# Kernel optimization log

Measured on AMD Instinct MI355X. Metric: run time of the kernel, lower is better.

Reference implementation:

```python
import jax, jax.numpy as jnp
import numpy as np

N = 50000
E = 400000
IN_DIM = 256
H1 = 512
H2 = 128
P_DROP = 0.5


def setup_inputs() -> dict:
    key = jax.random.key(0)
    ks = jax.random.split(key, 8)
    x = jax.random.normal(ks[0], (N, IN_DIM), dtype=jnp.float32)
    edge_index = jax.random.randint(ks[1], (2, E), 0, N, dtype=jnp.int64)
    W1 = jax.random.normal(ks[2], (IN_DIM, H1), dtype=jnp.float32) * (1.0 / np.sqrt(IN_DIM))
    b1 = jnp.zeros((H1,), dtype=jnp.float32)
    W2 = jax.random.normal(ks[3], (H1, H2), dtype=jnp.float32) * (1.0 / np.sqrt(H1))
    b2 = jnp.zeros((H2,), dtype=jnp.float32)
    a = jnp.full((1,), 0.25, dtype=jnp.float32)  # PReLU default init
    mask1 = jax.random.bernoulli(ks[4], 1.0 - P_DROP, (N, H1))
    mask2 = jax.random.bernoulli(ks[5], 1.0 - P_DROP, (N, H2))
    return {"x": x, "edge_index": edge_index, "W1": W1, "b1": b1,
            "W2": W2, "b2": b2, "a": a, "mask1": mask1, "mask2": mask2}


def reference(x, edge_index, W1, b1, W2, b2, a, mask1, mask2):
    n = x.shape[0]
    loop = jnp.arange(n, dtype=edge_index.dtype)
    src = jnp.concatenate([edge_index[0], loop])  # [E+N] with self-loops
    dst = jnp.concatenate([edge_index[1], loop])
    # symmetric normalization: deg^-1/2[src] * deg^-1/2[dst]
    deg = jax.ops.segment_sum(jnp.ones(src.shape[0], x.dtype), dst, num_segments=n)
    dis = jnp.where(deg > 0, jax.lax.rsqrt(jnp.maximum(deg, 1.0)), 0.0)
    norm = dis[src] * dis[dst]  # [E+N]

    scale = 1.0 / (1.0 - P_DROP)

    def gcn_conv(h, W, b):
        h = h @ W                               # dense transform [n, out]
        msg = h[src] * norm[:, None]            # gather + normalize [E+N, out]
        return jax.ops.segment_sum(msg, dst, num_segments=n) + b

    def prelu_dropout(h, mask):
        h = jnp.where(h >= 0, h, a * h)         # PReLU (shared scalar a)
        return jnp.where(mask, h * scale, 0.0)  # dropout p=0.5

    feat1 = prelu_dropout(gcn_conv(x, W1, b1), mask1)
    feat2 = prelu_dropout(gcn_conv(feat1, W2, b2), mask2)
    return feat2
```

## Files before the change

kernel.cpp:

```cpp
#include <hip/hip_runtime.h>
#include <hip/hip_bf16.h>

#define IN_DIM 256
#define H1 512
#define H2 128
#define BM 128
#define BKK 64
#define LDT 72
#define SCAN_CHUNK 4096

typedef unsigned short u16;
typedef unsigned long long u64;
typedef __attribute__((ext_vector_type(8))) short short8;
typedef __attribute__((ext_vector_type(4))) float floatx4;

__device__ __forceinline__ u16 f2bf(float f) {
    union { float f; unsigned u; } c; c.f = f;
    unsigned u = c.u;
    return (u16)((u + 0x7fffu + ((u >> 16) & 1u)) >> 16);
}
__device__ __forceinline__ float bflo(unsigned w) {
    union { unsigned u; float f; } c; c.u = w << 16; return c.f;
}
__device__ __forceinline__ float bfhi(unsigned w) {
    union { unsigned u; float f; } c; c.u = w & 0xffff0000u; return c.f;
}


__global__ __launch_bounds__(256) void pack_mask_kernel(const int4* __restrict__ mask4,
        u64* __restrict__ bits, int total4) {
    int gid = blockIdx.x * blockDim.x + threadIdx.x;
    int lane = threadIdx.x & 63;
    int4 v = (gid < total4) ? mask4[gid] : make_int4(0, 0, 0, 0);
    u64 b0 = __ballot(v.x != 0);
    u64 b1 = __ballot(v.y != 0);
    u64 b2 = __ballot(v.z != 0);
    u64 b3 = __ballot(v.w != 0);
    u64 sel = (lane == 0) ? b0 : (lane == 1) ? b1 : (lane == 2) ? b2 : b3;
    if (lane < 4 && gid < total4)
        bits[(size_t)(gid >> 6) * 4 + lane] = sel;
}


__global__ void hist_kernel(const int* __restrict__ dstA, int* __restrict__ counts,
                            int E, int n) {
    int e = blockIdx.x * blockDim.x + threadIdx.x;
    if (e < E) {
        int d = dstA[e];
        if ((unsigned)d < (unsigned)n) atomicAdd(&counts[d], 1);
    }
}


__global__ __launch_bounds__(256) void partial_sum_kernel(const int* __restrict__ counts,
        int* __restrict__ partials, int n) {
    int t = threadIdx.x;
    int base = blockIdx.x * SCAN_CHUNK + t * 16;
    int s = 0;
    int m = (base < n) ? min(16, n - base) : 0;
    for (int i = 0; i < m; ++i) s += counts[base + i];
    __shared__ int red[256];
    red[t] = s;
    __syncthreads();
    for (int off = 128; off > 0; off >>= 1) {
        if (t < off) red[t] += red[t + off];
        __syncthreads();
    }
    if (t == 0) partials[blockIdx.x] = red[0];
}

__global__ void scan_partials_kernel(int* __restrict__ partials, int nb) {
    if (threadIdx.x == 0 && blockIdx.x == 0) {
        int run = 0;
        for (int i = 0; i < nb; ++i) { int c = partials[i]; partials[i] = run; run += c; }
        partials[nb] = run;
    }
}

__global__ __launch_bounds__(256) void scan_emit_kernel(const int* __restrict__ counts,
        const int* __restrict__ partials, int* __restrict__ row_start,
        int* __restrict__ cursor, float* __restrict__ dis, int n, int nb) {
    int t = threadIdx.x;
    int base = blockIdx.x * SCAN_CHUNK + t * 16;
    int cnt[16];
    int s = 0;
    int m = (base < n) ? min(16, n - base) : 0;
    for (int i = 0; i < m; ++i) { cnt[i] = counts[base + i]; s += cnt[i]; }
    __shared__ int red[256];
    red[t] = s;
    __syncthreads();
    for (int off = 1; off < 256; off <<= 1) {
        int v = red[t];
        int vo = (t >= off) ? red[t - off] : 0;
        __syncthreads();
        red[t] = v + vo;
        __syncthreads();
    }
    int run = partials[blockIdx.x] + (t ? red[t - 1] : 0);
    for (int i = 0; i < m; ++i) {
        int c = cnt[i];
        row_start[base + i] = run;
        cursor[base + i] = run;
        dis[base + i] = rsqrtf((float)(c + 1));
        run += c;
    }
    if (blockIdx.x == 0 && t == 0) row_start[n] = partials[nb];
}

__global__ void scatter_kernel(const int* __restrict__ srcA, const int* __restrict__ dstA,
                               int* __restrict__ cursor, int* __restrict__ csr,
                               int E, int n) {
    int e = blockIdx.x * blockDim.x + threadIdx.x;
    if (e < E) {
        int d = dstA[e];
        int s = srcA[e];
        if ((unsigned)d < (unsigned)n && (unsigned)s < (unsigned)n) {
            int p = atomicAdd(&cursor[d], 1);
            csr[p] = s;
        }
    }
}

__global__ void scale_cast_kernel(const float* __restrict__ x, const float* __restrict__ dis,
                                  u16* __restrict__ xs, int n) {
    int gid = blockIdx.x * blockDim.x + threadIdx.x;
    int total = n * (IN_DIM / 4);
    if (gid >= total) return;
    int node = gid >> 6;
    float4 v = ((const float4*)x)[gid];
    float d = dis[node];
    uint2 o;
    o.x = (unsigned)f2bf(v.x * d) | ((unsigned)f2bf(v.y * d) << 16);
    o.y = (unsigned)f2bf(v.z * d) | ((unsigned)f2bf(v.w * d) << 16);
    ((uint2*)xs)[gid] = o;
}

__global__ void transpose_cast_kernel(const float* __restrict__ W, u16* __restrict__ Wt,
                                      int K, int Ncols) {
    int idx = blockIdx.x * blockDim.x + threadIdx.x;
    if (idx >= K * Ncols) return;
    int k = idx / Ncols, c = idx - k * Ncols;
    Wt[c * K + k] = f2bf(W[idx]);
}


__global__ __launch_bounds__(256) void agg1_kernel(const u16* __restrict__ xs,
        const int* __restrict__ row_start, const int* __restrict__ csr,
        const float* __restrict__ dis, u16* __restrict__ aggx, int n) {
    int gid = blockIdx.x * blockDim.x + threadIdx.x;
    int w = gid >> 6, lane = gid & 63;
    if (w >= n) return;
    const uint2* base = (const uint2*)xs;
    uint2 v = base[(size_t)w * 64 + lane];
    float a0 = bflo(v.x), a1 = bfhi(v.x), a2 = bflo(v.y), a3 = bfhi(v.y);
    int b = row_start[w], e = row_start[w + 1];
    int i = b;
    for (; i + 4 <= e; i += 4) {
        int s0 = csr[i], s1 = csr[i + 1], s2 = csr[i + 2], s3 = csr[i + 3];
        uint2 u0 = base[(size_t)s0 * 64 + lane];
        uint2 u1 = base[(size_t)s1 * 64 + lane];
        uint2 u2 = base[(size_t)s2 * 64 + lane];
        uint2 u3 = base[(size_t)s3 * 64 + lane];
        a0 += (bflo(u0.x) + bflo(u1.x)) + (bflo(u2.x) + bflo(u3.x));
        a1 += (bfhi(u0.x) + bfhi(u1.x)) + (bfhi(u2.x) + bfhi(u3.x));
        a2 += (bflo(u0.y) + bflo(u1.y)) + (bflo(u2.y) + bflo(u3.y));
        a3 += (bfhi(u0.y) + bfhi(u1.y)) + (bfhi(u2.y) + bfhi(u3.y));
    }
    for (; i < e; ++i) {
        int s = csr[i];
        uint2 u = base[(size_t)s * 64 + lane];
        a0 += bflo(u.x); a1 += bfhi(u.x); a2 += bflo(u.y); a3 += bfhi(u.y);
    }
    float dd = dis[w];
    uint2 o;
    o.x = (unsigned)f2bf(a0 * dd) | ((unsigned)f2bf(a1 * dd) << 16);
    o.y = (unsigned)f2bf(a2 * dd) | ((unsigned)f2bf(a3 * dd) << 16);
    ((uint2*)aggx)[(size_t)w * 64 + lane] = o;
}


__global__ __launch_bounds__(256) void gemm1_kernel(const u16* __restrict__ A,
        const u16* __restrict__ Bt, const float* __restrict__ bias,
        const float* __restrict__ a_p, const u64* __restrict__ mbits,
        u16* __restrict__ out, int M) {
    const int K = IN_DIM;
    __shared__ __align__(16) u16 As[BM * LDT];
    __shared__ __align__(16) u16 Bs[BM * LDT];
    int tid = threadIdx.x;
    int wave = tid >> 6, lane = tid & 63;
    int quad = lane >> 4, l16 = lane & 15;
    int wm = wave & 1, wn = wave >> 1;
    int m0 = blockIdx.x * BM, n0 = blockIdx.y * BM;

    floatx4 acc[4][4];
#pragma unroll
    for (int i = 0; i < 4; i++)
#pragma unroll
        for (int j = 0; j < 4; j++) acc[i][j] = (floatx4){0.f, 0.f, 0.f, 0.f};

    for (int k0 = 0; k0 < K; k0 += BKK) {
        __syncthreads();
#pragma unroll
        for (int u = tid; u < 1024; u += 256) {
            int row = u >> 3, seg = u & 7;
            uint4 av = make_uint4(0, 0, 0, 0);
            int gr = m0 + row;
            if (gr < M) av = *(const uint4*)&A[(size_t)gr * K + k0 + seg * 8];
            *(uint4*)&As[row * LDT + seg * 8] = av;
            uint4 bv = *(const uint4*)&Bt[(size_t)(n0 + row) * K + k0 + seg * 8];
            *(uint4*)&Bs[row * LDT + seg * 8] = bv;
        }
        __syncthreads();
        short8 bf8[4][2];
#pragma unroll
        for (int i = 0; i < 4; i++)
#pragma unroll
            for (int ks = 0; ks < 2; ks++)
                bf8[i][ks] = *(const short8*)&Bs[(wn * 64 + i * 16 + l16) * LDT + ks * 32 + quad * 8];
#pragma unroll
        for (int mt = 0; mt < 4; mt++) {
            short8 af0 = *(const short8*)&As[(wm * 64 + mt * 16 + l16) * LDT + quad * 8];
            short8 af1 = *(const short8*)&As[(wm * 64 + mt * 16 + l16) * LDT + 32 + quad * 8];
#pragma unroll
            for (int nt = 0; nt < 4; nt++) {
                acc[mt][nt] = __builtin_amdgcn_mfma_f32_16x16x32_bf16(
                    af0, bf8[nt][0], acc[mt][nt], 0, 0, 0);
                acc[mt][nt] = __builtin_amdgcn_mfma_f32_16x16x32_bf16(
                    af1, bf8[nt][1], acc[mt][nt], 0, 0, 0);
            }
        }
    }

    u64* mb = (u64*)As;
    __syncthreads();
    for (int u = tid; u < BM * 4; u += 256) {
        int row = u >> 2, j = u & 3;
        int gr = m0 + row;
        u64 val = 0;
        if (gr < M) val = mbits[(size_t)gr * 8 + (n0 >> 8) * 4 + j];
        mb[row * 5 + j] = val;
    }
    __syncthreads();

    float alpha = a_p[0];
#pragma unroll
    for (int mt = 0; mt < 4; mt++) {
#pragma unroll
        for (int r = 0; r < 4; r++) {
            int lr = wm * 64 + mt * 16 + quad * 4 + r;
            int row = m0 + lr;
            if (row >= M) continue;
#pragma unroll
            for (int nt = 0; nt < 4; nt++) {
                int c64 = nt * 16 + l16;
                int col = n0 + wn * 64 + c64;
                float v = acc[mt][nt][r] + bias[col];
                v = (v >= 0.f) ? v : alpha * v;
                u64 w = mb[lr * 5 + (l16 & 3)];
                int bit = ((n0 >> 2) + wn * 16 + nt * 4 + (l16 >> 2)) & 63;
                v = ((w >> bit) & 1ull) ? v * 2.0f : 0.0f;
                out[(size_t)row * H1 + col] = f2bf(v);
            }
        }
    }
}


__global__ __launch_bounds__(256) void gemm2_kernel(const u16* __restrict__ A,
        const u16* __restrict__ Bt, const float* __restrict__ dis,
        u16* __restrict__ out, int M) {
    const int K = H1;
    __shared__ __align__(16) u16 As[64 * LDT];
    __shared__ __align__(16) u16 Bs[128 * LDT];
    int tid = threadIdx.x;
    int wave = tid >> 6, lane = tid & 63;
    int quad = lane >> 4, l16 = lane & 15;
    int wm = wave & 1, wn = wave >> 1;
    int m0 = blockIdx.x * 64;

    floatx4 acc[2][4];
#pragma unroll
    for (int i = 0; i < 2; i++)
#pragma unroll
        for (int j = 0; j < 4; j++) acc[i][j] = (floatx4){0.f, 0.f, 0.f, 0.f};

    for (int k0 = 0; k0 < K; k0 += BKK) {
        __syncthreads();
#pragma unroll
        for (int u = tid; u < 1536; u += 256) {
            if (u < 512) {
                int row = u >> 3, seg = u & 7;
                uint4 av = make_uint4(0, 0, 0, 0);
                int gr = m0 + row;
                if (gr < M) av = *(const uint4*)&A[(size_t)gr * K + k0 + seg * 8];
                *(uint4*)&As[row * LDT + seg * 8] = av;
            } else {
                int v2 = u - 512;
                int row = v2 >> 3, seg = v2 & 7;
                uint4 bv = *(const uint4*)&Bt[(size_t)row * K + k0 + seg * 8];
                *(uint4*)&Bs[row * LDT + seg * 8] = bv;
            }
        }
        __syncthreads();
        short8 bf8[4][2];
#pragma unroll
        for (int i = 0; i < 4; i++)
#pragma unroll
            for (int ks = 0; ks < 2; ks++)
                bf8[i][ks] = *(const short8*)&Bs[(wn * 64 + i * 16 + l16) * LDT + ks * 32 + quad * 8];
#pragma unroll
        for (int mt = 0; mt < 2; mt++) {
            short8 af0 = *(const short8*)&As[(wm * 32 + mt * 16 + l16) * LDT + quad * 8];
            short8 af1 = *(const short8*)&As[(wm * 32 + mt * 16 + l16) * LDT + 32 + quad * 8];
#pragma unroll
            for (int nt = 0; nt < 4; nt++) {
                acc[mt][nt] = __builtin_amdgcn_mfma_f32_16x16x32_bf16(
                    af0, bf8[nt][0], acc[mt][nt], 0, 0, 0);
                acc[mt][nt] = __builtin_amdgcn_mfma_f32_16x16x32_bf16(
                    af1, bf8[nt][1], acc[mt][nt], 0, 0, 0);
            }
        }
    }

#pragma unroll
    for (int mt = 0; mt < 2; mt++) {
#pragma unroll
        for (int r = 0; r < 4; r++) {
            int row = m0 + wm * 32 + mt * 16 + quad * 4 + r;
            if (row >= M) continue;
            float dd = dis[row];
#pragma unroll
            for (int nt = 0; nt < 4; nt++) {
                int col = wn * 64 + nt * 16 + l16;
                out[(size_t)row * H2 + col] = f2bf(acc[mt][nt][r] * dd);
            }
        }
    }
}


__global__ __launch_bounds__(256) void agg2_kernel(const u16* __restrict__ ts,
        const int* __restrict__ row_start, const int* __restrict__ csr,
        const float* __restrict__ dis, const float* __restrict__ b2,
        const float* __restrict__ a_p, const int* __restrict__ mask,
        float* __restrict__ out, int n) {
    int gid = blockIdx.x * blockDim.x + threadIdx.x;
    int w = gid >> 6, lane = gid & 63;
    if (w >= n) return;
    const unsigned* base = (const unsigned*)ts;
    unsigned v = base[(size_t)w * 64 + lane];
    float a0 = bflo(v), a1 = bfhi(v);
    int b = row_start[w], e = row_start[w + 1];
    int i = b;
    for (; i + 4 <= e; i += 4) {
        int s0 = csr[i], s1 = csr[i + 1], s2 = csr[i + 2], s3 = csr[i + 3];
        unsigned u0 = base[(size_t)s0 * 64 + lane];
        unsigned u1 = base[(size_t)s1 * 64 + lane];
        unsigned u2 = base[(size_t)s2 * 64 + lane];
        unsigned u3 = base[(size_t)s3 * 64 + lane];
        a0 += (bflo(u0) + bflo(u1)) + (bflo(u2) + bflo(u3));
        a1 += (bfhi(u0) + bfhi(u1)) + (bfhi(u2) + bfhi(u3));
    }
    for (; i < e; ++i) {
        int s = csr[i];
        unsigned u = base[(size_t)s * 64 + lane];
        a0 += bflo(u); a1 += bfhi(u);
    }
    float dd = dis[w];
    float alpha = a_p[0];
    int c0 = lane * 2;
    float v0 = dd * a0 + b2[c0];
    float v1 = dd * a1 + b2[c0 + 1];
    v0 = (v0 >= 0.f) ? v0 : alpha * v0;
    v1 = (v1 >= 0.f) ? v1 : alpha * v1;
    int2 m = ((const int2*)mask)[(size_t)w * 64 + lane];
    v0 = m.x ? v0 * 2.f : 0.f;
    v1 = m.y ? v1 * 2.f : 0.f;
    ((float2*)out)[(size_t)w * 64 + lane] = make_float2(v0, v1);
}


extern "C" void kernel_launch(void* const* d_in, const int* in_sizes, int n_in,
                              void* d_out, int out_size, void* d_ws, size_t ws_size,
                              hipStream_t stream) {
    const float* x  = (const float*)d_in[0];
    const int* ei   = (const int*)d_in[1];
    const float* W1 = (const float*)d_in[2];
    const float* b1 = (const float*)d_in[3];
    const float* W2 = (const float*)d_in[4];
    const float* b2 = (const float*)d_in[5];
    const float* ap = (const float*)d_in[6];
    const int* mask1 = (const int*)d_in[7];
    const int* mask2 = (const int*)d_in[8];

    int n = in_sizes[0] / IN_DIM;
    int E = in_sizes[1] / 2;
    const int* srcA = ei;
    const int* dstA = ei + E;

    char* p = (char*)d_ws;
    auto alloc = [&](size_t bytes) {
        char* r = p;
        p += (bytes + 255) & ~(size_t)255;
        return r;
    };
    u16* feat1     = (u16*)alloc((size_t)n * H1 * 2);
    u16* xs        = feat1;
    u16* ts        = (u16*)alloc((size_t)n * H2 * 2);
    u64* bits1     = (u64*)ts;
    u16* w1t       = (u16*)alloc((size_t)IN_DIM * H1 * 2);
    u16* w2t       = (u16*)alloc((size_t)H1 * H2 * 2);
    float* dis     = (float*)alloc((size_t)n * 4);
    int* counts    = (int*)alloc((size_t)n * 4);
    int* cursor    = (int*)alloc((size_t)n * 4);
    int* row_start = (int*)alloc(((size_t)n + 1) * 4);
    int* csr       = (int*)alloc((size_t)E * 4);
    int nscan = (n + SCAN_CHUNK - 1) / SCAN_CHUNK;
    int* partials  = (int*)alloc(((size_t)nscan + 1) * 4);
    u16* aggx      = (u16*)d_out;
    if ((size_t)(p - (char*)d_ws) > ws_size) return;

    const int tpb = 256;
    int total4 = n * H1 / 4;
    hipMemsetAsync(counts, 0, (size_t)n * 4, stream);
    pack_mask_kernel<<<(total4 + tpb - 1) / tpb, tpb, 0, stream>>>((const int4*)mask1,
        bits1, total4);
    hist_kernel<<<(E + tpb - 1) / tpb, tpb, 0, stream>>>(dstA, counts, E, n);
    partial_sum_kernel<<<nscan, tpb, 0, stream>>>(counts, partials, n);
    scan_partials_kernel<<<1, 64, 0, stream>>>(partials, nscan);
    scan_emit_kernel<<<nscan, tpb, 0, stream>>>(counts, partials, row_start, cursor, dis, n, nscan);
    scatter_kernel<<<(E + tpb - 1) / tpb, tpb, 0, stream>>>(srcA, dstA, cursor, csr, E, n);
    scale_cast_kernel<<<((n * (IN_DIM / 4)) + tpb - 1) / tpb, tpb, 0, stream>>>(x, dis, xs, n);
    transpose_cast_kernel<<<((IN_DIM * H1) + tpb - 1) / tpb, tpb, 0, stream>>>(W1, w1t, IN_DIM, H1);
    transpose_cast_kernel<<<((H1 * H2) + tpb - 1) / tpb, tpb, 0, stream>>>(W2, w2t, H1, H2);
    agg1_kernel<<<(n * 64 + tpb - 1) / tpb, tpb, 0, stream>>>(xs, row_start, csr, dis, aggx, n);
    dim3 g1((n + BM - 1) / BM, H1 / BM);
    gemm1_kernel<<<g1, tpb, 0, stream>>>(aggx, w1t, b1, ap, bits1, feat1, n);
    dim3 g2((n + 63) / 64, 1);
    gemm2_kernel<<<g2, tpb, 0, stream>>>(feat1, w2t, dis, ts, n);
    agg2_kernel<<<(n * 64 + tpb - 1) / tpb, tpb, 0, stream>>>(ts, row_start, csr, dis, b2, ap,
                                                              mask2, (float*)d_out, n);
}
```

Baseline: 416.5 us.

## Split waves across two edges with wider gathers; pad CSR rows to even length

Both aggregation kernels now have each half-wave gather a different neighbor row. Lanes use 16-byte (agg1) or 8-byte (agg2) loads, and the two halves are combined with a cross-half shuffle at the end. To support this, every CSR row is padded to an even length, with the pad entry pointing at an extra all-zero row appended to the bf16 feature buffers. Separately, mask packing, the degree histogram and both weight transpose-casts are merged into one multi-role prep kernel to cut launch count. The risk is the extra padded gathers and the half-wave store path.

```diff
diff --git a/kernel.cpp b/kernel.cpp
--- a/kernel.cpp
+++ b/kernel.cpp
@@ -27,27 +27,42 @@
 }
 
 
-__global__ __launch_bounds__(256) void pack_mask_kernel(const int4* __restrict__ mask4,
-        u64* __restrict__ bits, int total4) {
-    int gid = blockIdx.x * blockDim.x + threadIdx.x;
-    int lane = threadIdx.x & 63;
-    int4 v = (gid < total4) ? mask4[gid] : make_int4(0, 0, 0, 0);
-    u64 b0 = __ballot(v.x != 0);
-    u64 b1 = __ballot(v.y != 0);
-    u64 b2 = __ballot(v.z != 0);
-    u64 b3 = __ballot(v.w != 0);
-    u64 sel = (lane == 0) ? b0 : (lane == 1) ? b1 : (lane == 2) ? b2 : b3;
-    if (lane < 4 && gid < total4)
-        bits[(size_t)(gid >> 6) * 4 + lane] = sel;
-}
-
-
-__global__ void hist_kernel(const int* __restrict__ dstA, int* __restrict__ counts,
-                            int E, int n) {
-    int e = blockIdx.x * blockDim.x + threadIdx.x;
-    if (e < E) {
-        int d = dstA[e];
-        if ((unsigned)d < (unsigned)n) atomicAdd(&counts[d], 1);
+__global__ __launch_bounds__(256) void prep_kernel(const int4* __restrict__ mask4,
+        u64* __restrict__ bits, int total4,
+        const int* __restrict__ dstA, int* __restrict__ counts, int E, int n,
+        const float* __restrict__ W1, u16* __restrict__ w1t,
+        const float* __restrict__ W2, u16* __restrict__ w2t,
+        int PB, int HB, int T1B) {
+    int b = blockIdx.x;
+    if (b < PB) {
+        int gid = b * 256 + threadIdx.x;
+        int lane = threadIdx.x & 63;
+        int4 v = (gid < total4) ? mask4[gid] : make_int4(0, 0, 0, 0);
+        u64 b0 = __ballot(v.x != 0);
+        u64 b1 = __ballot(v.y != 0);
+        u64 b2 = __ballot(v.z != 0);
+        u64 b3 = __ballot(v.w != 0);
+        u64 sel = (lane == 0) ? b0 : (lane == 1) ? b1 : (lane == 2) ? b2 : b3;
+        if (lane < 4 && gid < total4)
+            bits[(size_t)(gid >> 6) * 4 + lane] = sel;
+    } else if (b < PB + HB) {
+        int e = (b - PB) * 256 + threadIdx.x;
+        if (e < E) {
+            int d = dstA[e];
+            if ((unsigned)d < (unsigned)n) atomicAdd(&counts[d], 1);
+        }
+    } else if (b < PB + HB + T1B) {
+        int idx = (b - PB - HB) * 256 + threadIdx.x;
+        if (idx < IN_DIM * H1) {
+            int k = idx >> 9, c = idx & (H1 - 1);
+            w1t[c * IN_DIM + k] = f2bf(W1[idx]);
+        }
+    } else {
+        int idx = (b - PB - HB - T1B) * 256 + threadIdx.x;
+        if (idx < H1 * H2) {
+            int k = idx >> 7, c = idx & (H2 - 1);
+            w2t[c * H1 + k] = f2bf(W2[idx]);
+        }
     }
 }
 
@@ -58,7 +73,7 @@
     int base = blockIdx.x * SCAN_CHUNK + t * 16;
     int s = 0;
     int m = (base < n) ? min(16, n - base) : 0;
-    for (int i = 0; i < m; ++i) s += counts[base + i];
+    for (int i = 0; i < m; ++i) s += (counts[base + i] + 1) & ~1;
     __shared__ int red[256];
     red[t] = s;
     __syncthreads();
@@ -69,8 +84,11 @@
     if (t == 0) partials[blockIdx.x] = red[0];
 }
 
-__global__ void scan_partials_kernel(int* __restrict__ partials, int nb) {
-    if (threadIdx.x == 0 && blockIdx.x == 0) {
+__global__ void scan_partials_kernel(int* __restrict__ partials, int nb,
+                                     unsigned* __restrict__ ts_zero_row) {
+    int t = threadIdx.x;
+    if (t < 64) ts_zero_row[t] = 0;
+    if (t == 0 && blockIdx.x == 0) {
         int run = 0;
         for (int i = 0; i < nb; ++i) { int c = partials[i]; partials[i] = run; run += c; }
         partials[nb] = run;
@@ -79,13 +97,14 @@
 
 __global__ __launch_bounds__(256) void scan_emit_kernel(const int* __restrict__ counts,
         const int* __restrict__ partials, int* __restrict__ row_start,
-        int* __restrict__ cursor, float* __restrict__ dis, int n, int nb) {
+        int* __restrict__ cursor, float* __restrict__ dis,
+        int* __restrict__ csr, int n, int nb) {
     int t = threadIdx.x;
     int base = blockIdx.x * SCAN_CHUNK + t * 16;
     int cnt[16];
     int s = 0;
     int m = (base < n) ? min(16, n - base) : 0;
-    for (int i = 0; i < m; ++i) { cnt[i] = counts[base + i]; s += cnt[i]; }
+    for (int i = 0; i < m; ++i) { cnt[i] = counts[base + i]; s += (cnt[i] + 1) & ~1; }
     __shared__ int red[256];
     red[t] = s;
     __syncthreads();
@@ -102,7 +121,8 @@
         row_start[base + i] = run;
         cursor[base + i] = run;
         dis[base + i] = rsqrtf((float)(c + 1));
-        run += c;
+        if (c & 1) csr[run + c] = n;
+        run += (c + 1) & ~1;
     }
     if (blockIdx.x == 0 && t == 0) row_start[n] = partials[nb];
 }
@@ -124,23 +144,17 @@
 __global__ void scale_cast_kernel(const float* __restrict__ x, const float* __restrict__ dis,
                                   u16* __restrict__ xs, int n) {
     int gid = blockIdx.x * blockDim.x + threadIdx.x;
-    int total = n * (IN_DIM / 4);
+    int total = (n + 1) * (IN_DIM / 4);
     if (gid >= total) return;
     int node = gid >> 6;
-    float4 v = ((const float4*)x)[gid];
-    float d = dis[node];
-    uint2 o;
-    o.x = (unsigned)f2bf(v.x * d) | ((unsigned)f2bf(v.y * d) << 16);
-    o.y = (unsigned)f2bf(v.z * d) | ((unsigned)f2bf(v.w * d) << 16);
+    uint2 o = make_uint2(0, 0);
+    if (node < n) {
+        float4 v = ((const float4*)x)[gid];
+        float d = dis[node];
+        o.x = (unsigned)f2bf(v.x * d) | ((unsigned)f2bf(v.y * d) << 16);
+        o.y = (unsigned)f2bf(v.z * d) | ((unsigned)f2bf(v.w * d) << 16);
+    }
     ((uint2*)xs)[gid] = o;
-}
-
-__global__ void transpose_cast_kernel(const float* __restrict__ W, u16* __restrict__ Wt,
-                                      int K, int Ncols) {
-    int idx = blockIdx.x * blockDim.x + threadIdx.x;
-    if (idx >= K * Ncols) return;
-    int k = idx / Ncols, c = idx - k * Ncols;
-    Wt[c * K + k] = f2bf(W[idx]);
 }
 
 
@@ -150,32 +164,51 @@
     int gid = blockIdx.x * blockDim.x + threadIdx.x;
     int w = gid >> 6, lane = gid & 63;
     if (w >= n) return;
-    const uint2* base = (const uint2*)xs;
-    uint2 v = base[(size_t)w * 64 + lane];
-    float a0 = bflo(v.x), a1 = bfhi(v.x), a2 = bflo(v.y), a3 = bfhi(v.y);
+    const uint4* base = (const uint4*)xs;
+    int half = lane >> 5, hl = lane & 31;
+    float a0 = 0.f, a1 = 0.f, a2 = 0.f, a3 = 0.f, a4 = 0.f, a5 = 0.f, a6 = 0.f, a7 = 0.f;
+    if (half == 0) {
+        uint4 u = base[(size_t)w * 32 + hl];
+        a0 = bflo(u.x); a1 = bfhi(u.x); a2 = bflo(u.y); a3 = bfhi(u.y);
+        a4 = bflo(u.z); a5 = bfhi(u.z); a6 = bflo(u.w); a7 = bfhi(u.w);
+    }
     int b = row_start[w], e = row_start[w + 1];
     int i = b;
-    for (; i + 4 <= e; i += 4) {
-        int s0 = csr[i], s1 = csr[i + 1], s2 = csr[i + 2], s3 = csr[i + 3];
-        uint2 u0 = base[(size_t)s0 * 64 + lane];
-        uint2 u1 = base[(size_t)s1 * 64 + lane];
-        uint2 u2 = base[(size_t)s2 * 64 + lane];
-        uint2 u3 = base[(size_t)s3 * 64 + lane];
+    for (; i + 8 <= e; i += 8) {
+        int s0 = csr[i + half],     s1 = csr[i + 2 + half];
+        int s2 = csr[i + 4 + half], s3 = csr[i + 6 + half];
+        uint4 u0 = base[(size_t)s0 * 32 + hl];
+        uint4 u1 = base[(size_t)s1 * 32 + hl];
+        uint4 u2 = base[(size_t)s2 * 32 + hl];
+        uint4 u3 = base[(size_t)s3 * 32 + hl];
         a0 += (bflo(u0.x) + bflo(u1.x)) + (bflo(u2.x) + bflo(u3.x));
         a1 += (bfhi(u0.x) + bfhi(u1.x)) + (bfhi(u2.x) + bfhi(u3.x));
         a2 += (bflo(u0.y) + bflo(u1.y)) + (bflo(u2.y) + bflo(u3.y));
         a3 += (bfhi(u0.y) + bfhi(u1.y)) + (bfhi(u2.y) + bfhi(u3.y));
-    }
-    for (; i < e; ++i) {
-        int s = csr[i];
-        uint2 u = base[(size_t)s * 64 + lane];
+        a4 += (bflo(u0.z) + bflo(u1.z)) + (bflo(u2.z) + bflo(u3.z));
+        a5 += (bfhi(u0.z) + bfhi(u1.z)) + (bfhi(u2.z) + bfhi(u3.z));
+        a6 += (bflo(u0.w) + bflo(u1.w)) + (bflo(u2.w) + bflo(u3.w));
+        a7 += (bfhi(u0.w) + bfhi(u1.w)) + (bfhi(u2.w) + bfhi(u3.w));
+    }
+    for (; i < e; i += 2) {
+        int s = csr[i + half];
+        uint4 u = base[(size_t)s * 32 + hl];
         a0 += bflo(u.x); a1 += bfhi(u.x); a2 += bflo(u.y); a3 += bfhi(u.y);
-    }
-    float dd = dis[w];
-    uint2 o;
-    o.x = (unsigned)f2bf(a0 * dd) | ((unsigned)f2bf(a1 * dd) << 16);
-    o.y = (unsigned)f2bf(a2 * dd) | ((unsigned)f2bf(a3 * dd) << 16);
-    ((uint2*)aggx)[(size_t)w * 64 + lane] = o;
+        a4 += bflo(u.z); a5 += bfhi(u.z); a6 += bflo(u.w); a7 += bfhi(u.w);
+    }
+    a0 += __shfl_xor(a0, 32); a1 += __shfl_xor(a1, 32);
+    a2 += __shfl_xor(a2, 32); a3 += __shfl_xor(a3, 32);
+    a4 += __shfl_xor(a4, 32); a5 += __shfl_xor(a5, 32);
+    a6 += __shfl_xor(a6, 32); a7 += __shfl_xor(a7, 32);
+    if (half == 0) {
+        float dd = dis[w];
+        uint4 o;
+        o.x = (unsigned)f2bf(a0 * dd) | ((unsigned)f2bf(a1 * dd) << 16);
+        o.y = (unsigned)f2bf(a2 * dd) | ((unsigned)f2bf(a3 * dd) << 16);
+        o.z = (unsigned)f2bf(a4 * dd) | ((unsigned)f2bf(a5 * dd) << 16);
+        o.w = (unsigned)f2bf(a6 * dd) | ((unsigned)f2bf(a7 * dd) << 16);
+        ((uint4*)aggx)[(size_t)w * 32 + hl] = o;
+    }
 }
 
 
@@ -347,36 +380,53 @@
     int gid = blockIdx.x * blockDim.x + threadIdx.x;
     int w = gid >> 6, lane = gid & 63;
     if (w >= n) return;
-    const unsigned* base = (const unsigned*)ts;
-    unsigned v = base[(size_t)w * 64 + lane];
-    float a0 = bflo(v), a1 = bfhi(v);
+    const uint2* base = (const uint2*)ts;
+    int half = lane >> 5, hl = lane & 31;
+    float a0 = 0.f, a1 = 0.f, a2 = 0.f, a3 = 0.f;
+    if (half == 0) {
+        uint2 u = base[(size_t)w * 32 + hl];
+        a0 = bflo(u.x); a1 = bfhi(u.x); a2 = bflo(u.y); a3 = bfhi(u.y);
+    }
     int b = row_start[w], e = row_start[w + 1];
     int i = b;
-    for (; i + 4 <= e; i += 4) {
-        int s0 = csr[i], s1 = csr[i + 1], s2 = csr[i + 2], s3 = csr[i + 3];
-        unsigned u0 = base[(size_t)s0 * 64 + lane];
-        unsigned u1 = base[(size_t)s1 * 64 + lane];
-        unsigned u2 = base[(size_t)s2 * 64 + lane];
-        unsigned u3 = base[(size_t)s3 * 64 + lane];
-        a0 += (bflo(u0) + bflo(u1)) + (bflo(u2) + bflo(u3));
-        a1 += (bfhi(u0) + bfhi(u1)) + (bfhi(u2) + bfhi(u3));
-    }
-    for (; i < e; ++i) {
-        int s = csr[i];
-        unsigned u = base[(size_t)s * 64 + lane];
-        a0 += bflo(u); a1 += bfhi(u);
-    }
-    float dd = dis[w];
-    float alpha = a_p[0];
-    int c0 = lane * 2;
-    float v0 = dd * a0 + b2[c0];
-    float v1 = dd * a1 + b2[c0 + 1];
-    v0 = (v0 >= 0.f) ? v0 : alpha * v0;
-    v1 = (v1 >= 0.f) ? v1 : alpha * v1;
-    int2 m = ((const int2*)mask)[(size_t)w * 64 + lane];
-    v0 = m.x ? v0 * 2.f : 0.f;
-    v1 = m.y ? v1 * 2.f : 0.f;
-    ((float2*)out)[(size_t)w * 64 + lane] = make_float2(v0, v1);
+    for (; i + 8 <= e; i += 8) {
+        int s0 = csr[i + half],     s1 = csr[i + 2 + half];
+        int s2 = csr[i + 4 + half], s3 = csr[i + 6 + half];
+        uint2 u0 = base[(size_t)s0 * 32 + hl];
+        uint2 u1 = base[(size_t)s1 * 32 + hl];
+        uint2 u2 = base[(size_t)s2 * 32 + hl];
+        uint2 u3 = base[(size_t)s3 * 32 + hl];
+        a0 += (bflo(u0.x) + bflo(u1.x)) + (bflo(u2.x) + bflo(u3.x));
+        a1 += (bfhi(u0.x) + bfhi(u1.x)) + (bfhi(u2.x) + bfhi(u3.x));
+        a2 += (bflo(u0.y) + bflo(u1.y)) + (bflo(u2.y) + bflo(u3.y));
+        a3 += (bfhi(u0.y) + bfhi(u1.y)) + (bfhi(u2.y) + bfhi(u3.y));
+    }
+    for (; i < e; i += 2) {
+        int s = csr[i + half];
+        uint2 u = base[(size_t)s * 32 + hl];
+        a0 += bflo(u.x); a1 += bfhi(u.x); a2 += bflo(u.y); a3 += bfhi(u.y);
+    }
+    a0 += __shfl_xor(a0, 32); a1 += __shfl_xor(a1, 32);
+    a2 += __shfl_xor(a2, 32); a3 += __shfl_xor(a3, 32);
+    if (half == 0) {
+        float dd = dis[w];
+        float alpha = a_p[0];
+        float4 bb = ((const float4*)b2)[hl];
+        float v0 = dd * a0 + bb.x;
+        float v1 = dd * a1 + bb.y;
+        float v2 = dd * a2 + bb.z;
+        float v3 = dd * a3 + bb.w;
+        v0 = (v0 >= 0.f) ? v0 : alpha * v0;
+        v1 = (v1 >= 0.f) ? v1 : alpha * v1;
+        v2 = (v2 >= 0.f) ? v2 : alpha * v2;
+        v3 = (v3 >= 0.f) ? v3 : alpha * v3;
+        int4 m = ((const int4*)mask)[(size_t)w * 32 + hl];
+        v0 = m.x ? v0 * 2.f : 0.f;
+        v1 = m.y ? v1 * 2.f : 0.f;
+        v2 = m.z ? v2 * 2.f : 0.f;
+        v3 = m.w ? v3 * 2.f : 0.f;
+        ((float4*)out)[(size_t)w * 32 + hl] = make_float4(v0, v1, v2, v3);
+    }
 }
 
 
@@ -406,7 +456,7 @@
     };
     u16* feat1     = (u16*)alloc((size_t)n * H1 * 2);
     u16* xs        = feat1;
-    u16* ts        = (u16*)alloc((size_t)n * H2 * 2);
+    u16* ts        = (u16*)alloc((size_t)(n + 1) * H2 * 2);
     u64* bits1     = (u64*)ts;
     u16* w1t       = (u16*)alloc((size_t)IN_DIM * H1 * 2);
     u16* w2t       = (u16*)alloc((size_t)H1 * H2 * 2);
@@ -414,7 +464,7 @@
     int* counts    = (int*)alloc((size_t)n * 4);
     int* cursor    = (int*)alloc((size_t)n * 4);
     int* row_start = (int*)alloc(((size_t)n + 1) * 4);
-    int* csr       = (int*)alloc((size_t)E * 4);
+    int* csr       = (int*)alloc(((size_t)E + n + 64) * 4);
     int nscan = (n + SCAN_CHUNK - 1) / SCAN_CHUNK;
     int* partials  = (int*)alloc(((size_t)nscan + 1) * 4);
     u16* aggx      = (u16*)d_out;
@@ -422,17 +472,20 @@
 
     const int tpb = 256;
     int total4 = n * H1 / 4;
+    int PB = (total4 + tpb - 1) / tpb;
+    int HB = (E + tpb - 1) / tpb;
+    int T1B = (IN_DIM * H1 + tpb - 1) / tpb;
+    int T2B = (H1 * H2 + tpb - 1) / tpb;
     hipMemsetAsync(counts, 0, (size_t)n * 4, stream);
-    pack_mask_kernel<<<(total4 + tpb - 1) / tpb, tpb, 0, stream>>>((const int4*)mask1,
-        bits1, total4);
-    hist_kernel<<<(E + tpb - 1) / tpb, tpb, 0, stream>>>(dstA, counts, E, n);
+    prep_kernel<<<PB + HB + T1B + T2B, tpb, 0, stream>>>((const int4*)mask1, bits1, total4,
+        dstA, counts, E, n, W1, w1t, W2, w2t, PB, HB, T1B);
     partial_sum_kernel<<<nscan, tpb, 0, stream>>>(counts, partials, n);
-    scan_partials_kernel<<<1, 64, 0, stream>>>(partials, nscan);
-    scan_emit_kernel<<<nscan, tpb, 0, stream>>>(counts, partials, row_start, cursor, dis, n, nscan);
+    scan_partials_kernel<<<1, 64, 0, stream>>>(partials, nscan,
+        (unsigned*)(ts + (size_t)n * H2));
+    scan_emit_kernel<<<nscan, tpb, 0, stream>>>(counts, partials, row_start, cursor, dis,
+                                                csr, n, nscan);
     scatter_kernel<<<(E + tpb - 1) / tpb, tpb, 0, stream>>>(srcA, dstA, cursor, csr, E, n);
-    scale_cast_kernel<<<((n * (IN_DIM / 4)) + tpb - 1) / tpb, tpb, 0, stream>>>(x, dis, xs, n);
-    transpose_cast_kernel<<<((IN_DIM * H1) + tpb - 1) / tpb, tpb, 0, stream>>>(W1, w1t, IN_DIM, H1);
-    transpose_cast_kernel<<<((H1 * H2) + tpb - 1) / tpb, tpb, 0, stream>>>(W2, w2t, H1, H2);
+    scale_cast_kernel<<<(((n + 1) * (IN_DIM / 4)) + tpb - 1) / tpb, tpb, 0, stream>>>(x, dis, xs, n);
     agg1_kernel<<<(n * 64 + tpb - 1) / tpb, tpb, 0, stream>>>(xs, row_start, csr, dis, aggx, n);
     dim3 g1((n + BM - 1) / BM, H1 / BM);
     gemm1_kernel<<<g1, tpb, 0, stream>>>(aggx, w1t, b1, ap, bits1, feat1, n);
```

Measured after the change: 408.4 us, median of 3. Within noise of the previous version (-1.9%).
